# Performance work log

Measured on AMD Instinct MI355X. Metric: run time of the kernel, lower is better.

The kernel has to match this reference:

```python
import jax, jax.numpy as jnp
import numpy as np

D_MODEL = 2048
NUM_HEADS = 16
HEAD_DIM = D_MODEL // NUM_HEADS
SEQ = 2048
BATCH = 2
ROPE_BASE = 10000.0
EPS = 1e-5


def _rope_cache(seq_len, head_dim, base):
    inv_freq = 1.0 / (base ** (jnp.arange(0, head_dim, 2, dtype=jnp.float32) / head_dim))
    t = jnp.arange(seq_len, dtype=jnp.float32)
    freqs = jnp.outer(t, inv_freq)                      # [S, hd/2]
    emb = jnp.concatenate([freqs, freqs], axis=-1)      # [S, hd]
    return jnp.cos(emb), jnp.sin(emb)


def _rotate_half(x):
    x1, x2 = jnp.split(x, 2, axis=-1)
    return jnp.concatenate([-x2, x1], axis=-1)


def setup_inputs() -> dict:
    key = jax.random.key(0)
    ks = jax.random.split(key, 8)
    s = 1.0 / np.sqrt(D_MODEL)
    inp = {
        "x": jax.random.normal(ks[0], (SEQ, BATCH, D_MODEL), dtype=jnp.float32),
        "causal_mask": jnp.triu(jnp.ones((SEQ, SEQ), dtype=jnp.bool_), k=1),
        "key_padding_mask": jnp.zeros((BATCH, SEQ), dtype=jnp.bool_),
        "norm_w": jnp.ones((D_MODEL,), dtype=jnp.float32),
        "q_w": jax.random.normal(ks[1], (D_MODEL, D_MODEL), dtype=jnp.float32) * s,
        "q_b": jnp.zeros((D_MODEL,), dtype=jnp.float32),
        "k_w": jax.random.normal(ks[2], (D_MODEL, D_MODEL), dtype=jnp.float32) * s,
        "k_b": jnp.zeros((D_MODEL,), dtype=jnp.float32),
        "v_w": jax.random.normal(ks[3], (D_MODEL, D_MODEL), dtype=jnp.float32) * s,
        "v_b": jnp.zeros((D_MODEL,), dtype=jnp.float32),
        "o_w": jax.random.normal(ks[4], (D_MODEL, D_MODEL), dtype=jnp.float32) * s,
        "o_b": jnp.zeros((D_MODEL,), dtype=jnp.float32),
    }
    return inp


def reference(x, causal_mask, key_padding_mask, norm_w, q_w, q_b, k_w, k_b, v_w, v_b, o_w, o_b):
    seq_len, batch, _ = x.shape
    # RMSNorm variant: x / (||x||_2 + eps) * w  (note: L2 norm, not RMS)
    nrm = jnp.linalg.norm(x, axis=-1, keepdims=True)
    xn = x / (nrm + EPS) * norm_w

    q = (xn @ q_w.T + q_b).reshape(seq_len, batch, NUM_HEADS, HEAD_DIM)
    k = (xn @ k_w.T + k_b).reshape(seq_len, batch, NUM_HEADS, HEAD_DIM)
    v = (xn @ v_w.T + v_b).reshape(seq_len, batch, NUM_HEADS, HEAD_DIM)

    cos, sin = _rope_cache(seq_len, HEAD_DIM, ROPE_BASE)
    cos = cos[:, None, None, :]
    sin = sin[:, None, None, :]
    q = q * cos + _rotate_half(q) * sin
    k = k * cos + _rotate_half(k) * sin

    # [S,B,H,D] -> [B,H,S,D]
    q = q.transpose(1, 2, 0, 3)
    k = k.transpose(1, 2, 0, 3)
    v = v.transpose(1, 2, 0, 3)

    scores = jnp.einsum('bhqd,bhkd->bhqk', q, k) / jnp.sqrt(jnp.float32(HEAD_DIM))
    neg_inf = jnp.float32(-jnp.inf)
    scores = jnp.where(causal_mask[None, None, :, :], neg_inf, scores)
    scores = jnp.where(key_padding_mask[:, None, None, :], neg_inf, scores)

    attn = jax.nn.softmax(scores, axis=-1)
    out = jnp.einsum('bhqk,bhkd->bhqd', attn, v)
    out = out.transpose(2, 0, 1, 3).reshape(seq_len, batch, D_MODEL)  # [S,B,D]
    return out @ o_w.T + o_b
```

## Files before the change

kernel.cpp:

```cpp
#include <hip/hip_runtime.h>
#include <hip/hip_bf16.h>
#include <cstdint>

typedef __attribute__((ext_vector_type(8))) short short8_t;
typedef __attribute__((ext_vector_type(4))) short s16x4;
typedef __attribute__((ext_vector_type(4))) float f32x4;

#define SEQ 2048
#define BATCH 2
#define DM 2048
#define NH 16
#define HD 128
#define SCALE 0.08838834764831845f

__device__ __forceinline__ short f2bf(float f) {
    union { __hip_bfloat16 h; short s; } u; u.h = __float2bfloat16(f); return u.s;
}
__device__ __forceinline__ float bf2f(short s) {
    union { short s; __hip_bfloat16 h; } u; u.s = s; return __bfloat162float(u.h);
}

__global__ void __launch_bounds__(256) prep_kernel(const float* __restrict__ qw,
                                                   const float* __restrict__ kw,
                                                   const float* __restrict__ vw,
                                                   const float* __restrict__ ow,
                                                   short* __restrict__ wqkv,
                                                   const float* __restrict__ x,
                                                   const float* __restrict__ nw,
                                                   short* __restrict__ xn,
                                                   float* __restrict__ cosT,
                                                   float* __restrict__ sinT) {
    const int bid = blockIdx.x;
    const int t = threadIdx.x;
    if (bid < 2048) {
        const int per = DM * DM / 4;
        int i = bid * 256 + t;
        const int stride = 2048 * 256;
        for (; i < 4 * per; i += stride) {
            int region = i / per;
            int off = i - region * per;
            const float* src = region == 0 ? qw : (region == 1 ? kw : (region == 2 ? vw : ow));
            float4 v = ((const float4*)src)[off];
            s16x4 o;
            o[0] = f2bf(v.x); o[1] = f2bf(v.y); o[2] = f2bf(v.z); o[3] = f2bf(v.w);
            ((s16x4*)(wqkv + (size_t)region * DM * DM))[off] = o;
        }
    } else if (bid < 2560) {
        int j = (bid - 2048) * 256 + t;
        int tpos = j >> 6, i = j & 63;
        float inv = exp2f(-(2.0f * (float)i / 128.0f) * log2f(10000.0f));
        float a = (float)tpos * inv;
        cosT[tpos * 64 + i] = cosf(a);
        sinT[tpos * 64 + i] = sinf(a);
    } else {
        __shared__ float red[4];
        int row = bid - 2560;
        const float* xr = x + (size_t)row * DM;
        short* outr = xn + (size_t)row * DM;
        float vals[8];
        float ss = 0.f;
#pragma unroll
        for (int i = 0; i < 8; ++i) { float v = xr[t + 256 * i]; vals[i] = v; ss += v * v; }
#pragma unroll
        for (int off = 1; off < 64; off <<= 1) ss += __shfl_xor(ss, off);
        int lane = t & 63, wv = t >> 6;
        if (lane == 0) red[wv] = ss;
        __syncthreads();
        float tot = red[0] + red[1] + red[2] + red[3];
        float inv = 1.f / (sqrtf(tot) + 1e-5f);
#pragma unroll
        for (int i = 0; i < 8; ++i)
            outr[t + 256 * i] = f2bf(vals[i] * inv * nw[t + 256 * i]);
    }
}

__device__ __forceinline__ void stage64(const short* __restrict__ G, int gRow0, int K, int kb,
                                        short* dstLds, int w, int lane) {
#pragma unroll
    for (int p = 0; p < 4; ++p) {
        int c = p * 256 + w * 64 + lane;
        int row = c >> 3;
        int slot = (c & 7) ^ (row & 7);
        const short* g = G + (size_t)(gRow0 + row) * K + kb + slot * 8;
        __builtin_amdgcn_global_load_lds((const __attribute__((address_space(1))) void*)g,
                                         (__attribute__((address_space(3))) void*)(dstLds + (p * 256 + w * 64) * 8),
                                         16, 0, 0);
    }
}

template <int MODE>
__global__ void __launch_bounds__(256) gemm_bt2(const short* __restrict__ A,
                                                const short* __restrict__ B,
                                                int N, int K,
                                                short* __restrict__ oq, short* __restrict__ ok,
                                                short* __restrict__ ov,
                                                const float* __restrict__ bq,
                                                const float* __restrict__ bk,
                                                const float* __restrict__ bv,
                                                float* __restrict__ outF,
                                                const float* __restrict__ bias) {
    __shared__ short As[128 * 64];
    __shared__ short Bs[128 * 64];
    const int tid = threadIdx.x;
    const int lane = tid & 63;
    const int w = tid >> 6;
    const int wr = w >> 1, wc = w & 1;
    const int brow = blockIdx.y * 128;
    const int bcol = blockIdx.x * 128;

    f32x4 acc[4][4];
#pragma unroll
    for (int i = 0; i < 4; ++i)
#pragma unroll
        for (int j = 0; j < 4; ++j) acc[i][j] = (f32x4){0.f, 0.f, 0.f, 0.f};

    const int fr = lane & 15;
    const int fs = lane >> 4;

    for (int kb = 0; kb < K; kb += 64) {
        stage64(A, brow, K, kb, As, w, lane);
        stage64(B, bcol, K, kb, Bs, w, lane);
        __syncthreads();

        short8_t af[4][2], bfv[4][2];
#pragma unroll
        for (int i = 0; i < 4; ++i) {
            int ar = wr * 64 + i * 16 + fr;
#pragma unroll
            for (int ks = 0; ks < 2; ++ks)
                af[i][ks] = *(const short8_t*)&As[ar * 64 + ((ks * 4 + fs) ^ (fr & 7)) * 8];
        }
#pragma unroll
        for (int j = 0; j < 4; ++j) {
            int br = wc * 64 + j * 16 + fr;
#pragma unroll
            for (int ks = 0; ks < 2; ++ks)
                bfv[j][ks] = *(const short8_t*)&Bs[br * 64 + ((ks * 4 + fs) ^ (fr & 7)) * 8];
        }
#pragma unroll
        for (int ks = 0; ks < 2; ++ks)
#pragma unroll
            for (int i = 0; i < 4; ++i)
#pragma unroll
                for (int j = 0; j < 4; ++j)
                    acc[i][j] = __builtin_amdgcn_mfma_f32_16x16x32_bf16(af[i][ks], bfv[j][ks], acc[i][j], 0, 0, 0);
        __syncthreads();
    }

    const int fq = (lane >> 4) * 4;
#pragma unroll
    for (int i = 0; i < 4; ++i) {
        int mrow = brow + wr * 64 + i * 16 + fq;
#pragma unroll
        for (int j = 0; j < 4; ++j) {
            int ncol = bcol + wc * 64 + j * 16 + fr;
            if (MODE == 0) {
                int which = ncol >> 11;
                int hl = ncol & 2047;
                int h = hl >> 7, d = hl & 127;
                const float* bp = which == 0 ? bq : (which == 1 ? bk : bv);
                short* dst = which == 0 ? oq : (which == 1 ? ok : ov);
                float bval = bp[hl];
#pragma unroll
                for (int jj = 0; jj < 4; ++jj) {
                    int m = mrow + jj;
                    int s = m >> 1, b = m & 1;
                    float v = acc[i][j][jj] + bval;
                    size_t idx;
                    if (which == 2)
                        idx = (((size_t)(b * NH + h)) * HD + d) * SEQ + s;
                    else
                        idx = (((size_t)(b * NH + h)) * SEQ + s) * HD + d;
                    dst[idx] = f2bf(v);
                }
            } else {
                float bval = bias[ncol];
#pragma unroll
                for (int jj = 0; jj < 4; ++jj) {
                    int m = mrow + jj;
                    outF[(size_t)m * N + ncol] = acc[i][j][jj] + bval;
                }
            }
        }
    }
}

__global__ void __launch_bounds__(256) rope_kernel(short* __restrict__ q, short* __restrict__ k,
                                                   const float* __restrict__ cosT,
                                                   const float* __restrict__ sinT) {
    int w = threadIdx.x >> 6, lane = threadIdx.x & 63;
    int idx = blockIdx.x * 4 + w;
    int s = idx & (SEQ - 1);
    size_t base = (size_t)idx * HD;
    float c = cosT[s * 64 + lane], sn = sinT[s * 64 + lane];
    float q1 = bf2f(q[base + lane]), q2 = bf2f(q[base + lane + 64]);
    q[base + lane] = f2bf((q1 * c - q2 * sn) * SCALE);
    q[base + lane + 64] = f2bf((q2 * c + q1 * sn) * SCALE);
    float k1 = bf2f(k[base + lane]), k2 = bf2f(k[base + lane + 64]);
    k[base + lane] = f2bf(k1 * c - k2 * sn);
    k[base + lane + 64] = f2bf(k2 * c + k1 * sn);
}

__global__ void __launch_bounds__(512) attn_kernel(const short* __restrict__ Q,
                                                   const short* __restrict__ K,
                                                   const short* __restrict__ V,
                                                   short* __restrict__ AO) {
    __shared__ short Kl[64 * 136];
    __shared__ short Vt[128 * 88];
    __shared__ short Pl[8][16 * 88];

    const int bh = blockIdx.x;
    const int qt = blockIdx.y;
    const int b = bh >> 4;
    const int h = bh & 15;
    const size_t base = (size_t)bh * (SEQ * HD);
    const int tid = threadIdx.x;
    const int lane = tid & 63;
    const int w = tid >> 6;
    const int fr = lane & 15;
    const int fk = (lane >> 4) * 8;
    const int fq = (lane >> 4) * 4;
    const int qbase = qt * 128 + w * 16;
    const int qg = qbase + fr;

    const int kr = tid >> 4;
    const int kc8 = (tid & 15) * 8;
    const int vd = tid >> 3;
    const int vc8 = (tid & 7) * 8;

    short8_t qf[4];
#pragma unroll
    for (int kc = 0; kc < 4; ++kc)
        qf[kc] = *(const short8_t*)&Q[base + (size_t)(qbase + fr) * HD + kc * 32 + fk];

    f32x4 acc[8];
#pragma unroll
    for (int dt = 0; dt < 8; ++dt) acc[dt] = (f32x4){0.f, 0.f, 0.f, 0.f};
    float m_r = -1e30f, l_r = 0.f;

    const int ktmax = qt * 2 + 1;

    short8_t kreg[2], vreg[2];
#pragma unroll
    for (int p = 0; p < 2; ++p) {
        kreg[p] = *(const short8_t*)&K[base + (size_t)(p * 32 + kr) * HD + kc8];
        vreg[p] = *(const short8_t*)&V[base + (size_t)(p * 64 + vd) * SEQ + vc8];
    }
#pragma unroll
    for (int p = 0; p < 2; ++p) {
        *(short8_t*)&Kl[(p * 32 + kr) * 136 + kc8] = kreg[p];
        *(short8_t*)&Vt[(p * 64 + vd) * 88 + vc8] = vreg[p];
    }
    __syncthreads();

    for (int kt = 0; kt <= ktmax; ++kt) {
        const bool active = (kt * 64 <= qbase + 15);
        f32x4 st[4];
        if (active) {
            __builtin_amdgcn_s_setprio(1);
#pragma unroll
            for (int nt = 0; nt < 4; ++nt) {
                f32x4 a = (f32x4){0.f, 0.f, 0.f, 0.f};
#pragma unroll
                for (int kc = 0; kc < 4; ++kc) {
                    short8_t kf = *(const short8_t*)&Kl[(nt * 16 + fr) * 136 + kc * 32 + fk];
                    a = __builtin_amdgcn_mfma_f32_16x16x32_bf16(kf, qf[kc], a, 0, 0, 0);
                }
                st[nt] = a;
            }
            __builtin_amdgcn_s_setprio(0);
        }

        if (kt < ktmax) {
            const size_t kb2 = base + (size_t)((kt + 1) * 64) * HD;
            const size_t vb2 = base + (size_t)(kt + 1) * 64;
#pragma unroll
            for (int p = 0; p < 2; ++p) {
                kreg[p] = *(const short8_t*)&K[kb2 + (size_t)(p * 32 + kr) * HD + kc8];
                vreg[p] = *(const short8_t*)&V[vb2 + (size_t)(p * 64 + vd) * SEQ + vc8];
            }
        }

        if (active) {
            const bool needMask = (kt * 64 + 63 > qbase);
            float rmax = -1e30f;
            if (needMask) {
#pragma unroll
                for (int nt = 0; nt < 4; ++nt)
#pragma unroll
                    for (int jj = 0; jj < 4; ++jj) {
                        int kg = kt * 64 + nt * 16 + fq + jj;
                        float sv = st[nt][jj];
                        sv = (kg > qg) ? -1e30f : sv;
                        st[nt][jj] = sv;
                        rmax = fmaxf(rmax, sv);
                    }
            } else {
#pragma unroll
                for (int nt = 0; nt < 4; ++nt)
#pragma unroll
                    for (int jj = 0; jj < 4; ++jj) rmax = fmaxf(rmax, st[nt][jj]);
            }
            rmax = fmaxf(rmax, __shfl_xor(rmax, 16));
            rmax = fmaxf(rmax, __shfl_xor(rmax, 32));

            const bool doRescale = !(m_r > -1e29f && __all(rmax - m_r <= 8.0f));
            float m_new = doRescale ? fmaxf(m_r, rmax) : m_r;
            float rsum = 0.f;
#pragma unroll
            for (int nt = 0; nt < 4; ++nt) {
                s16x4 pk;
#pragma unroll
                for (int jj = 0; jj < 4; ++jj) {
                    float p = __expf(st[nt][jj] - m_new);
                    rsum += p;
                    pk[jj] = f2bf(p);
                }
                *(s16x4*)&Pl[w][fr * 88 + nt * 16 + fq] = pk;
            }
            rsum += __shfl_xor(rsum, 16);
            rsum += __shfl_xor(rsum, 32);
            if (doRescale) {
                float corr = __expf(m_r - m_new);
                l_r = l_r * corr + rsum;
                m_r = m_new;
                float c4[4];
#pragma unroll
                for (int jj = 0; jj < 4; ++jj) c4[jj] = __shfl(corr, fq + jj);
#pragma unroll
                for (int dt = 0; dt < 8; ++dt)
#pragma unroll
                    for (int jj = 0; jj < 4; ++jj) acc[dt][jj] *= c4[jj];
            } else {
                l_r += rsum;
            }

            __builtin_amdgcn_s_setprio(1);
#pragma unroll
            for (int kc = 0; kc < 2; ++kc) {
                short8_t pf = *(const short8_t*)&Pl[w][fr * 88 + kc * 32 + fk];
#pragma unroll
                for (int dt = 0; dt < 8; ++dt) {
                    short8_t vf = *(const short8_t*)&Vt[(dt * 16 + fr) * 88 + kc * 32 + fk];
                    acc[dt] = __builtin_amdgcn_mfma_f32_16x16x32_bf16(pf, vf, acc[dt], 0, 0, 0);
                }
            }
            __builtin_amdgcn_s_setprio(0);
        }

        __syncthreads();
        if (kt < ktmax) {
#pragma unroll
            for (int p = 0; p < 2; ++p) {
                *(short8_t*)&Kl[(p * 32 + kr) * 136 + kc8] = kreg[p];
                *(short8_t*)&Vt[(p * 64 + vd) * 88 + vc8] = vreg[p];
            }
            __syncthreads();
        }
    }

    float linv[4];
#pragma unroll
    for (int jj = 0; jj < 4; ++jj) linv[jj] = 1.f / __shfl(l_r, fq + jj);
#pragma unroll
    for (int dt = 0; dt < 8; ++dt) {
#pragma unroll
        for (int jj = 0; jj < 4; ++jj) {
            int qrow = qbase + fq + jj;
            int d = dt * 16 + fr;
            AO[((size_t)(qrow * BATCH + b)) * DM + h * HD + d] = f2bf(acc[dt][jj] * linv[jj]);
        }
    }
}

extern "C" void kernel_launch(void* const* d_in, const int* in_sizes, int n_in,
                              void* d_out, int out_size, void* d_ws, size_t ws_size,
                              hipStream_t stream) {
    (void)in_sizes; (void)n_in; (void)out_size; (void)ws_size;
    const float* x  = (const float*)d_in[0];
    const float* nw = (const float*)d_in[3];
    const float* qw = (const float*)d_in[4];
    const float* qbias = (const float*)d_in[5];
    const float* kw = (const float*)d_in[6];
    const float* kbias = (const float*)d_in[7];
    const float* vw = (const float*)d_in[8];
    const float* vbias = (const float*)d_in[9];
    const float* ow = (const float*)d_in[10];
    const float* obias = (const float*)d_in[11];
    float* out = (float*)d_out;

    char* ws = (char*)d_ws;
    size_t off = 0;
    float* cosT = (float*)(ws + off); off += (size_t)SEQ * 64 * 4;
    float* sinT = (float*)(ws + off); off += (size_t)SEQ * 64 * 4;
    short* wqkv = (short*)(ws + off); off += (size_t)3 * DM * DM * 2;
    short* wo   = (short*)(ws + off); off += (size_t)DM * DM * 2;
    short* xn   = (short*)(ws + off); off += (size_t)SEQ * BATCH * DM * 2;
    short* qd   = (short*)(ws + off); off += (size_t)SEQ * BATCH * DM * 2;
    short* kd   = (short*)(ws + off); off += (size_t)SEQ * BATCH * DM * 2;
    short* vd   = (short*)(ws + off); off += (size_t)SEQ * BATCH * DM * 2;
    short* ao   = xn;

    prep_kernel<<<2560 + SEQ * BATCH, 256, 0, stream>>>(qw, kw, vw, ow, wqkv, x, nw, xn, cosT, sinT);
    gemm_bt2<0><<<dim3(3 * DM / 128, SEQ * BATCH / 128), 256, 0, stream>>>(
        xn, wqkv, 3 * DM, DM, qd, kd, vd, qbias, kbias, vbias, nullptr, nullptr);
    rope_kernel<<<BATCH * NH * SEQ / 4, 256, 0, stream>>>(qd, kd, cosT, sinT);
    attn_kernel<<<dim3(BATCH * NH, SEQ / 128), 512, 0, stream>>>(qd, kd, vd, ao);
    gemm_bt2<1><<<dim3(DM / 128, SEQ * BATCH / 128), 256, 0, stream>>>(
        ao, wo, DM, DM, nullptr, nullptr, nullptr, nullptr, nullptr, nullptr, out, obias);
}
```

Before: 280.5 us.

## Double-buffer GEMM LDS staging with async prefetch and fuse Q RoPE into attention

Rewrites the projection GEMM to use two LDS stages in dynamic shared memory, issuing global-to-LDS loads for the next K tile before computing on the current one, with explicit vmcnt waits, raw ds_read_b128 and priority raising around MFMAs. Q rotary embedding and scaling move into the attention kernel's Q fragment load, so the standalone rope pass only touches K. The change targets exposed load latency in the GEMM main loop and one extra read/write pass over Q. It doubles the GEMM's LDS footprint, which may reduce occupancy.

```diff
diff --git a/kernel.cpp b/kernel.cpp
--- a/kernel.cpp
+++ b/kernel.cpp
@@ -74,33 +74,20 @@
     }
 }
 
-__device__ __forceinline__ void stage64(const short* __restrict__ G, int gRow0, int K, int kb,
-                                        short* dstLds, int w, int lane) {
-#pragma unroll
-    for (int p = 0; p < 4; ++p) {
-        int c = p * 256 + w * 64 + lane;
-        int row = c >> 3;
-        int slot = (c & 7) ^ (row & 7);
-        const short* g = G + (size_t)(gRow0 + row) * K + kb + slot * 8;
-        __builtin_amdgcn_global_load_lds((const __attribute__((address_space(1))) void*)g,
-                                         (__attribute__((address_space(3))) void*)(dstLds + (p * 256 + w * 64) * 8),
-                                         16, 0, 0);
-    }
-}
+#define DSREAD(d, a) asm volatile("ds_read_b128 %0, %1" : "=v"(d) : "v"(a))
 
 template <int MODE>
-__global__ void __launch_bounds__(256) gemm_bt2(const short* __restrict__ A,
-                                                const short* __restrict__ B,
-                                                int N, int K,
-                                                short* __restrict__ oq, short* __restrict__ ok,
-                                                short* __restrict__ ov,
-                                                const float* __restrict__ bq,
-                                                const float* __restrict__ bk,
-                                                const float* __restrict__ bv,
-                                                float* __restrict__ outF,
-                                                const float* __restrict__ bias) {
-    __shared__ short As[128 * 64];
-    __shared__ short Bs[128 * 64];
+__global__ void __launch_bounds__(256) gemm_db(const short* __restrict__ A,
+                                               const short* __restrict__ B,
+                                               int N, int K,
+                                               short* __restrict__ oq, short* __restrict__ ok,
+                                               short* __restrict__ ov,
+                                               const float* __restrict__ bq,
+                                               const float* __restrict__ bk,
+                                               const float* __restrict__ bv,
+                                               float* __restrict__ outF,
+                                               const float* __restrict__ bias) {
+    extern __shared__ short lds[];
     const int tid = threadIdx.x;
     const int lane = tid & 63;
     const int w = tid >> 6;
@@ -108,6 +95,18 @@
     const int brow = blockIdx.y * 128;
     const int bcol = blockIdx.x * 128;
 
+    const short* gA[4]; const short* gB[4]; int ldsC[4];
+#pragma unroll
+    for (int p = 0; p < 4; ++p) {
+        int c = p * 256 + tid;
+        int row = c >> 3;
+        int slot = (c & 7) ^ (row & 7);
+        gA[p] = A + (size_t)(brow + row) * K + slot * 8;
+        gB[p] = B + (size_t)(bcol + row) * K + slot * 8;
+        ldsC[p] = c * 8;
+    }
+    const uint32_t ldsBase = (uint32_t)(uintptr_t)&lds[0];
+
     f32x4 acc[4][4];
 #pragma unroll
     for (int i = 0; i < 4; ++i)
@@ -116,27 +115,61 @@
 
     const int fr = lane & 15;
     const int fs = lane >> 4;
-
-    for (int kb = 0; kb < K; kb += 64) {
-        stage64(A, brow, K, kb, As, w, lane);
-        stage64(B, bcol, K, kb, Bs, w, lane);
-        __syncthreads();
-
+    uint32_t aOff[4][2], bOff[4][2];
+#pragma unroll
+    for (int i = 0; i < 4; ++i)
+#pragma unroll
+        for (int ks = 0; ks < 2; ++ks) {
+            int ch = (ks * 4 + fs) ^ (fr & 7);
+            int ar = wr * 64 + i * 16 + fr;
+            int br = wc * 64 + i * 16 + fr;
+            aOff[i][ks] = ldsBase + (uint32_t)(ar * 128 + ch * 16);
+            bOff[i][ks] = ldsBase + 32768u + (uint32_t)(br * 128 + ch * 16);
+        }
+
+    const int nt = K >> 6;
+#pragma unroll
+    for (int p = 0; p < 4; ++p)
+        __builtin_amdgcn_global_load_lds((const __attribute__((address_space(1))) void*)gA[p],
+                                         (__attribute__((address_space(3))) void*)(lds + ldsC[p]), 16, 0, 0);
+#pragma unroll
+    for (int p = 0; p < 4; ++p)
+        __builtin_amdgcn_global_load_lds((const __attribute__((address_space(1))) void*)gB[p],
+                                         (__attribute__((address_space(3))) void*)(lds + 16384 + ldsC[p]), 16, 0, 0);
+
+    for (int t = 0; t < nt; ++t) {
+        const int cur = t & 1;
+        if (t + 1 < nt) {
+            const int nb = (t + 1) & 1;
+            const int kb = (t + 1) << 6;
+#pragma unroll
+            for (int p = 0; p < 4; ++p)
+                __builtin_amdgcn_global_load_lds((const __attribute__((address_space(1))) void*)(gA[p] + kb),
+                                                 (__attribute__((address_space(3))) void*)(lds + nb * 8192 + ldsC[p]), 16, 0, 0);
+#pragma unroll
+            for (int p = 0; p < 4; ++p)
+                __builtin_amdgcn_global_load_lds((const __attribute__((address_space(1))) void*)(gB[p] + kb),
+                                                 (__attribute__((address_space(3))) void*)(lds + 16384 + nb * 8192 + ldsC[p]), 16, 0, 0);
+            asm volatile("s_waitcnt vmcnt(8)" ::: "memory");
+        } else {
+            asm volatile("s_waitcnt vmcnt(0)" ::: "memory");
+        }
+        __builtin_amdgcn_s_barrier();
+
+        const uint32_t ab = (uint32_t)(cur * 16384);
         short8_t af[4][2], bfv[4][2];
 #pragma unroll
-        for (int i = 0; i < 4; ++i) {
-            int ar = wr * 64 + i * 16 + fr;
-#pragma unroll
-            for (int ks = 0; ks < 2; ++ks)
-                af[i][ks] = *(const short8_t*)&As[ar * 64 + ((ks * 4 + fs) ^ (fr & 7)) * 8];
-        }
-#pragma unroll
-        for (int j = 0; j < 4; ++j) {
-            int br = wc * 64 + j * 16 + fr;
-#pragma unroll
-            for (int ks = 0; ks < 2; ++ks)
-                bfv[j][ks] = *(const short8_t*)&Bs[br * 64 + ((ks * 4 + fs) ^ (fr & 7)) * 8];
-        }
+        for (int i = 0; i < 4; ++i)
+#pragma unroll
+            for (int ks = 0; ks < 2; ++ks) DSREAD(af[i][ks], aOff[i][ks] + ab);
+#pragma unroll
+        for (int j = 0; j < 4; ++j)
+#pragma unroll
+            for (int ks = 0; ks < 2; ++ks) DSREAD(bfv[j][ks], bOff[j][ks] + ab);
+        asm volatile("s_waitcnt lgkmcnt(0)" ::: "memory");
+        __builtin_amdgcn_sched_barrier(0);
+
+        __builtin_amdgcn_s_setprio(1);
 #pragma unroll
         for (int ks = 0; ks < 2; ++ks)
 #pragma unroll
@@ -144,7 +177,8 @@
 #pragma unroll
                 for (int j = 0; j < 4; ++j)
                     acc[i][j] = __builtin_amdgcn_mfma_f32_16x16x32_bf16(af[i][ks], bfv[j][ks], acc[i][j], 0, 0, 0);
-        __syncthreads();
+        __builtin_amdgcn_s_setprio(0);
+        __builtin_amdgcn_s_barrier();
     }
 
     const int fq = (lane >> 4) * 4;
@@ -185,17 +219,14 @@
     }
 }
 
-__global__ void __launch_bounds__(256) rope_kernel(short* __restrict__ q, short* __restrict__ k,
-                                                   const float* __restrict__ cosT,
-                                                   const float* __restrict__ sinT) {
+__global__ void __launch_bounds__(256) rope_k_kernel(short* __restrict__ k,
+                                                     const float* __restrict__ cosT,
+                                                     const float* __restrict__ sinT) {
     int w = threadIdx.x >> 6, lane = threadIdx.x & 63;
     int idx = blockIdx.x * 4 + w;
     int s = idx & (SEQ - 1);
     size_t base = (size_t)idx * HD;
     float c = cosT[s * 64 + lane], sn = sinT[s * 64 + lane];
-    float q1 = bf2f(q[base + lane]), q2 = bf2f(q[base + lane + 64]);
-    q[base + lane] = f2bf((q1 * c - q2 * sn) * SCALE);
-    q[base + lane + 64] = f2bf((q2 * c + q1 * sn) * SCALE);
     float k1 = bf2f(k[base + lane]), k2 = bf2f(k[base + lane + 64]);
     k[base + lane] = f2bf(k1 * c - k2 * sn);
     k[base + lane + 64] = f2bf(k2 * c + k1 * sn);
@@ -204,6 +235,8 @@
 __global__ void __launch_bounds__(512) attn_kernel(const short* __restrict__ Q,
                                                    const short* __restrict__ K,
                                                    const short* __restrict__ V,
+                                                   const float* __restrict__ cosT,
+                                                   const float* __restrict__ sinT,
                                                    short* __restrict__ AO) {
     __shared__ short Kl[64 * 136];
     __shared__ short Vt[128 * 88];
@@ -231,7 +264,27 @@
     short8_t qf[4];
 #pragma unroll
     for (int kc = 0; kc < 4; ++kc)
-        qf[kc] = *(const short8_t*)&Q[base + (size_t)(qbase + fr) * HD + kc * 32 + fk];
+        qf[kc] = *(const short8_t*)&Q[base + (size_t)(qg) * HD + kc * 32 + fk];
+
+    {
+        const float* cb = cosT + (size_t)qg * 64;
+        const float* sb = sinT + (size_t)qg * 64;
+#pragma unroll
+        for (int kc = 0; kc < 2; ++kc) {
+            float4 c0 = *(const float4*)&cb[kc * 32 + fk];
+            float4 c1 = *(const float4*)&cb[kc * 32 + fk + 4];
+            float4 s0 = *(const float4*)&sb[kc * 32 + fk];
+            float4 s1 = *(const float4*)&sb[kc * 32 + fk + 4];
+            float cv[8] = {c0.x, c0.y, c0.z, c0.w, c1.x, c1.y, c1.z, c1.w};
+            float sv[8] = {s0.x, s0.y, s0.z, s0.w, s1.x, s1.y, s1.z, s1.w};
+#pragma unroll
+            for (int e = 0; e < 8; ++e) {
+                float q1 = bf2f(qf[kc][e]), q2 = bf2f(qf[kc + 2][e]);
+                qf[kc][e]     = f2bf((q1 * cv[e] - q2 * sv[e]) * SCALE);
+                qf[kc + 2][e] = f2bf((q2 * cv[e] + q1 * sv[e]) * SCALE);
+            }
+        }
+    }
 
     f32x4 acc[8];
 #pragma unroll
@@ -401,11 +454,14 @@
     short* vd   = (short*)(ws + off); off += (size_t)SEQ * BATCH * DM * 2;
     short* ao   = xn;
 
+    hipFuncSetAttribute((const void*)gemm_db<0>, hipFuncAttributeMaxDynamicSharedMemorySize, 65536);
+    hipFuncSetAttribute((const void*)gemm_db<1>, hipFuncAttributeMaxDynamicSharedMemorySize, 65536);
+
     prep_kernel<<<2560 + SEQ * BATCH, 256, 0, stream>>>(qw, kw, vw, ow, wqkv, x, nw, xn, cosT, sinT);
-    gemm_bt2<0><<<dim3(3 * DM / 128, SEQ * BATCH / 128), 256, 0, stream>>>(
+    gemm_db<0><<<dim3(3 * DM / 128, SEQ * BATCH / 128), 256, 65536, stream>>>(
         xn, wqkv, 3 * DM, DM, qd, kd, vd, qbias, kbias, vbias, nullptr, nullptr);
-    rope_kernel<<<BATCH * NH * SEQ / 4, 256, 0, stream>>>(qd, kd, cosT, sinT);
-    attn_kernel<<<dim3(BATCH * NH, SEQ / 128), 512, 0, stream>>>(qd, kd, vd, ao);
-    gemm_bt2<1><<<dim3(DM / 128, SEQ * BATCH / 128), 256, 0, stream>>>(
+    rope_k_kernel<<<BATCH * NH * SEQ / 4, 256, 0, stream>>>(kd, cosT, sinT);
+    attn_kernel<<<dim3(BATCH * NH, SEQ / 128), 512, 0, stream>>>(qd, kd, vd, cosT, sinT, ao);
+    gemm_db<1><<<dim3(DM / 128, SEQ * BATCH / 128), 256, 65536, stream>>>(
         ao, wo, DM, DM, nullptr, nullptr, nullptr, nullptr, nullptr, nullptr, out, obias);
 }
```

Result: faster. 259.7 us (-7.4%).
